# Optimization experiments

Measured on AMD Instinct MI355X. Metric: run time of the kernel, lower is better.

## Reference

```python
import jax, jax.numpy as jnp
import numpy as np

N_NODES = 20000
N_EDGES = 160000
DIM = 64          # node embedding dim
SUB = 16          # sub_dim
NB = 5            # n_bonds_type
RB = 8            # radial basis size (FeNNol default)
CUTOFF = 5.0
NLAYERS = 3
HID = 64          # conv_hidden
NSPEC = 86        # species onehot size
XI_SHAPE = RB * SUB * NB   # 640
FC_IN = XI_SHAPE + SUB     # 656
LOG2 = float(np.log(2.0))


def ssp(x):
    # shifted softplus activation
    return jax.nn.softplus(x) - jnp.asarray(LOG2, x.dtype)


def radial_bessel(r):
    # sine Bessel radial basis on [0, cutoff]; r: [E] -> [E, RB]
    n = jnp.arange(1, RB + 1, dtype=r.dtype)
    x = r[:, None]
    return jnp.sqrt(jnp.asarray(2.0 / CUTOFF, r.dtype)) * jnp.sin(n * jnp.pi * x / CUTOFF) / x


def setup_inputs() -> dict:
    key = jax.random.key(0)
    ks = jax.random.split(key, 16)
    inp = {}
    inp['species'] = jax.random.randint(ks[0], (N_NODES,), 1, NSPEC, dtype=jnp.int32)
    inp['edge_src'] = jnp.sort(jax.random.randint(ks[1], (N_EDGES,), 0, N_NODES, dtype=jnp.int32))
    inp['edge_dst'] = jax.random.randint(ks[2], (N_EDGES,), 0, N_NODES, dtype=jnp.int32)
    # distances kept away from 0 to keep 1/r finite
    inp['distances'] = jax.random.uniform(ks[3], (N_EDGES,), jnp.float32, 0.5, CUTOFF)
    inp['switch'] = jax.random.uniform(ks[4], (N_EDGES,), jnp.float32)
    inp['bond_order'] = jax.random.uniform(ks[5], (N_EDGES, NB), jnp.float32)
    s = lambda fan: 1.0 / np.sqrt(fan)
    inp['W_species'] = jax.random.normal(ks[6], (NSPEC, DIM), jnp.float32) * s(NSPEC)
    inp['Wl'] = jax.random.normal(ks[7], (NLAYERS, DIM, 2 * SUB), jnp.float32) * s(DIM)
    inp['bl'] = jnp.zeros((NLAYERS, 2 * SUB), jnp.float32)
    inp['fcW1'] = jax.random.normal(ks[8], (NLAYERS, FC_IN, HID), jnp.float32) * s(FC_IN)
    inp['fcb1'] = jnp.zeros((NLAYERS, HID), jnp.float32)
    inp['fcW2'] = jax.random.normal(ks[9], (NLAYERS, HID, HID), jnp.float32) * s(HID)
    inp['fcb2'] = jnp.zeros((NLAYERS, HID), jnp.float32)
    inp['fcW3'] = jax.random.normal(ks[10], (NLAYERS, HID, DIM), jnp.float32) * s(HID)
    inp['fcb3'] = jnp.zeros((NLAYERS, DIM), jnp.float32)
    return inp


def reference(species, edge_src, edge_dst, distances, switch, bond_order,
              W_species, Wl, bl, fcW1, fcb1, fcW2, fcb2, fcW3, fcb3):
    # onehot(species) @ W (no bias) == embedding gather
    xi = W_species[species]                      # [N, DIM]
    rb = radial_bessel(distances)                # [E, RB]
    sw = switch[:, None]                         # [E, 1]
    for l in range(NLAYERS):
        h = xi @ Wl[l] + bl[l]                   # [N, 2*SUB]
        si, mi = h[:, :SUB], h[:, SUB:]
        # per-edge outer product: [E, RB, SUB, NB] -> [E, RB*SUB*NB]
        xi_j = (rb[:, :, None, None]
                * mi[edge_dst][:, None, :, None]
                * bond_order[:, None, None, :]).reshape(N_EDGES, XI_SHAPE)
        dxi = jax.ops.segment_sum(xi_j * sw, edge_src, num_segments=N_NODES)  # [N, 640]
        dxi = jnp.concatenate([dxi, si], axis=-1)                             # [N, 656]
        dxi = ssp(dxi @ fcW1[l] + fcb1[l])
        dxi = ssp(dxi @ fcW2[l] + fcb2[l])
        dxi = dxi @ fcW3[l] + fcb3[l]            # last FC layer linear
        xi = xi + dxi
    return xi
```

## Files before the change

### kernel.cpp

```cpp
#include <hip/hip_runtime.h>
#include <math.h>

#define N_NODES 20000
#define N_EDGES 160000
#define EPAD    160256
#define NTILES  1250

#define PI_F 3.14159265358979323846f
#define LN2_F 0.69314718055994530942f

#define W1PK 43008
#define W23PK 4096
#define WPK_LAYER 51200
#define XROW 680
#define CAP 312
#define NFILL_MAX 272

#define NW_EDGE 626
#define NW_XI   625
#define NW_PACK 600
#define NW_ROW  79
#define NW_TOTAL (NW_EDGE + NW_XI + NW_PACK + NW_ROW)

typedef short short8v __attribute__((ext_vector_type(8)));
typedef float f32x4 __attribute__((ext_vector_type(4)));
typedef unsigned short u16;
typedef unsigned long long ull;

__device__ __forceinline__ float sspf(float x) {
    return fmaxf(x, 0.0f) + log1pf(expf(-fabsf(x))) - LN2_F;
}
__device__ __forceinline__ u16 f2bf(float f) {
    unsigned int u = __float_as_uint(f);
    return (u16)((u + 0x7fffu + ((u >> 16) & 1u)) >> 16);
}
__device__ __forceinline__ unsigned int pk2(float a, float b) {
    return (unsigned int)f2bf(a) | ((unsigned int)f2bf(b) << 16);
}
__device__ __forceinline__ ull mge(int t) {
    t = t < 0 ? 0 : (t > 4 ? 4 : t);
    return t == 4 ? 0ULL : (~0ULL << (t * 16));
}


__device__ void edge_wt_work(int blk, const float* __restrict__ dist,
                             const float* __restrict__ sw,
                             const float* __restrict__ bo,
                             u16* __restrict__ WT, char* smem)
{
    u16 (*tr)[264] = reinterpret_cast<u16(*)[264]>(smem);
    int tid = threadIdx.x;
    int e = blk * 256 + tid;

    if (e < N_EDGES) {
        float r = dist[e];
        float c = sqrtf(0.4f) / r * sw[e];
        float rbv[8];
        #pragma unroll
        for (int n = 0; n < 8; ++n)
            rbv[n] = c * sinf((float)(n + 1) * PI_F * r * 0.2f);
        float bov[5];
        #pragma unroll
        for (int b = 0; b < 5; ++b) bov[b] = bo[(size_t)e * 5 + b];
        #pragma unroll
        for (int n = 0; n < 8; ++n)
            #pragma unroll
            for (int b = 0; b < 5; ++b)
                tr[n * 5 + b][tid] = f2bf(rbv[n] * bov[b]);
    } else {
        #pragma unroll
        for (int j = 0; j < 40; ++j) tr[j][tid] = 0;
    }
    __syncthreads();

    #pragma unroll
    for (int i = 0; i < 5; ++i) {
        int qq = tid + i * 256;
        int s = qq >> 5, c = qq & 31;
        uint4 v = *reinterpret_cast<const uint4*>(&tr[s][c * 8]);
        *reinterpret_cast<uint4*>(WT + (size_t)s * EPAD + blk * 256 + c * 8) = v;
    }
}

__device__ void row_start_work(int blk, const int* __restrict__ src,
                               int* __restrict__ row)
{
    int i = blk * 256 + threadIdx.x;
    if (i > N_NODES) return;
    int lo = 0, hi = N_EDGES;
    while (lo < hi) {
        int mid = (lo + hi) >> 1;
        if (src[mid] < i) lo = mid + 1; else hi = mid;
    }
    row[i] = lo;
}

__device__ void pack_w_work(int blk, const float* __restrict__ fcW1,
                            const float* __restrict__ fcW2,
                            const float* __restrict__ fcW3,
                            u16* __restrict__ Wpk)
{
    int idx = blk * 256 + threadIdx.x;
    if (idx >= 3 * WPK_LAYER) return;
    int layer = idx / WPK_LAYER;
    int r = idx - layer * WPK_LAYER;
    float val = 0.0f;
    if (r < W1PK) {
        int e = r;
        int j = e & 7, lane = (e >> 3) & 63, c16 = (e >> 9) & 3, ks = e >> 11;
        int k = ks * 32 + (lane >> 4) * 8 + j;
        int colm = c16 * 16 + (lane & 15);
        if (k < 640) {
            int nbv = k >> 4, ss = k & 15;
            int nn = nbv / 5, bb = nbv - nn * 5;
            val = fcW1[(size_t)layer * 656 * 64 + (size_t)(nn * 80 + ss * 5 + bb) * 64 + colm];
        } else if (k < 656) {
            val = fcW1[(size_t)layer * 656 * 64 + (size_t)k * 64 + colm];
        }
    } else {
        bool is2 = (r < W1PK + W23PK);
        const float* W = is2 ? fcW2 : fcW3;
        int e = is2 ? (r - W1PK) : (r - W1PK - W23PK);
        int j = e & 7, lane = (e >> 3) & 63, c16 = (e >> 9) & 3, ks = e >> 11;
        int k = ks * 32 + (lane >> 4) * 8 + j;
        int colm = c16 * 16 + (lane & 15);
        val = W[(size_t)layer * 64 * 64 + (size_t)k * 64 + colm];
    }
    Wpk[(size_t)layer * WPK_LAYER + r] = f2bf(val);
}

__device__ void xi_init_h_work(int blk, const int* __restrict__ species,
                               const float* __restrict__ Wsp,
                               const float* __restrict__ Wl0,
                               const float* __restrict__ bl0,
                               float* __restrict__ xi,
                               float* __restrict__ h, char* smem)
{
    float* xs = reinterpret_cast<float*>(smem);
    float* ws = reinterpret_cast<float*>(smem + 8192);
    int tid = threadIdx.x;
    int nb = blk * 32;

    #pragma unroll
    for (int i = 0; i < 2; ++i) {
        int idx = tid + i * 256;
        int node = idx >> 4, c4 = idx & 15;
        int sp = species[nb + node];
        float4 v = reinterpret_cast<const float4*>(Wsp + (size_t)sp * 64)[c4];
        reinterpret_cast<float4*>(xs)[idx] = v;
        reinterpret_cast<float4*>(xi)[(size_t)(nb + node) * 16 + c4] = v;
    }
    {
        const float4* wsrc = reinterpret_cast<const float4*>(Wl0);
        float4* wd = reinterpret_cast<float4*>(ws);
        #pragma unroll
        for (int i = 0; i < 2; ++i) wd[tid + i * 256] = wsrc[tid + i * 256];
    }
    __syncthreads();

    int c4g = tid & 7;
    int nrow = tid >> 3;
    float4 acc = *reinterpret_cast<const float4*>(bl0 + c4g * 4);
    const float* xr = xs + nrow * 64;
    #pragma unroll 8
    for (int j = 0; j < 64; ++j) {
        float xv = xr[j];
        float4 wv = *reinterpret_cast<const float4*>(ws + j * 32 + c4g * 4);
        acc.x = fmaf(xv, wv.x, acc.x);
        acc.y = fmaf(xv, wv.y, acc.y);
        acc.z = fmaf(xv, wv.z, acc.z);
        acc.w = fmaf(xv, wv.w, acc.w);
    }
    *reinterpret_cast<float4*>(h + (size_t)(nb + nrow) * 32 + c4g * 4) = acc;
}

__global__ __launch_bounds__(256) void setup_kernel(
    const float* __restrict__ dist, const float* __restrict__ sw,
    const float* __restrict__ bo, u16* __restrict__ WT,
    const int* __restrict__ species, const float* __restrict__ Wsp,
    const float* __restrict__ Wl0, const float* __restrict__ bl0,
    float* __restrict__ xi, float* __restrict__ h0,
    const float* __restrict__ fcW1, const float* __restrict__ fcW2,
    const float* __restrict__ fcW3, u16* __restrict__ Wpk,
    const int* __restrict__ esrc, int* __restrict__ rowp)
{
    __shared__ __align__(16) char smem[21760];
    int wk = blockIdx.x;
    if (wk < NW_EDGE)
        edge_wt_work(wk, dist, sw, bo, WT, smem);
    else if (wk < NW_EDGE + NW_XI)
        xi_init_h_work(wk - NW_EDGE, species, Wsp, Wl0, bl0, xi, h0, smem);
    else if (wk < NW_EDGE + NW_XI + NW_PACK)
        pack_w_work(wk - NW_EDGE - NW_XI, fcW1, fcW2, fcW3, Wpk);
    else
        row_start_work(wk - NW_EDGE - NW_XI - NW_PACK, esrc, rowp);
}

__global__ __launch_bounds__(256) void agg_fc_fused(
    const u16* __restrict__ WT,
    const int* __restrict__ row,
    const int* __restrict__ dst,
    const float* __restrict__ h_in,
    float* __restrict__ h_out,
    const u16* __restrict__ Wpk,
    const float* __restrict__ b1,
    const float* __restrict__ b2,
    const float* __restrict__ b3,
    const float* __restrict__ Wl_next,
    const float* __restrict__ bl_next,
    int do_h,
    float* __restrict__ xi)
{
    __shared__ __align__(16) char smem[21760 + 16 * CAP * 2];
    u16 (*Xs)[XROW] = reinterpret_cast<u16(*)[XROW]>(smem);
    u16* mi  = reinterpret_cast<u16*>(smem + 21760);
    u16* Y1  = reinterpret_cast<u16*>(smem + 21760);
    u16* Y2  = reinterpret_cast<u16*>(smem + 21760 + 2304);
    float* Yo = reinterpret_cast<float*>(smem + 21760 + 4608);
    float* Wlds = reinterpret_cast<float*>(smem);
    float* Xn   = reinterpret_cast<float*>(smem + 8192);

    int tid = threadIdx.x;
    int wv = tid >> 6;
    int lane = tid & 63;
    int s = lane & 15;
    int kg = lane >> 4;
    int n0 = blockIdx.x * 16;
    int base = n0 + (wv << 2);

    int E0 = row[n0];
    int E1 = row[n0 + 16];
    int G0 = E0 & ~7;
    int nfill = E1 - G0;
    if (nfill > NFILL_MAX) nfill = NFILL_MAX;

    {
        int t = kg;
        u16* xr = &Xs[(wv << 2) + t][0];
        xr[640 + s] = f2bf(h_in[(size_t)(base + t) * 32 + s]);
        xr[656 + s] = 0;
    }

    for (int i = tid; i < nfill; i += 256) {
        int d = dst[G0 + i];
        const float4* hp = reinterpret_cast<const float4*>(h_in + (size_t)d * 32 + 16);
        float4 v0 = hp[0], v1 = hp[1], v2 = hp[2], v3 = hp[3];
        u16* col = mi + i;
        col[0 * CAP]  = f2bf(v0.x); col[1 * CAP]  = f2bf(v0.y);
        col[2 * CAP]  = f2bf(v0.z); col[3 * CAP]  = f2bf(v0.w);
        col[4 * CAP]  = f2bf(v1.x); col[5 * CAP]  = f2bf(v1.y);
        col[6 * CAP]  = f2bf(v1.z); col[7 * CAP]  = f2bf(v1.w);
        col[8 * CAP]  = f2bf(v2.x); col[9 * CAP]  = f2bf(v2.y);
        col[10 * CAP] = f2bf(v2.z); col[11 * CAP] = f2bf(v2.w);
        col[12 * CAP] = f2bf(v3.x); col[13 * CAP] = f2bf(v3.y);
        col[14 * CAP] = f2bf(v3.z); col[15 * CAP] = f2bf(v3.w);
    }
    __syncthreads();

    for (int t = 0; t < 4; ++t) {
        int node = base + t;
        int e0 = row[node], e1 = row[node + 1];
        int e0a = e0 & ~7;
        int L0 = e0a - G0;
        int nks = (e1 - e0a + 31) >> 5;

        f32x4 c0 = {0.f, 0.f, 0.f, 0.f};
        f32x4 c1 = {0.f, 0.f, 0.f, 0.f};
        f32x4 c2 = {0.f, 0.f, 0.f, 0.f};

        for (int kc = 0; kc < nks; ++kc) {
            int ebg = e0a + kc * 32 + kg * 8;
            int ebl = L0 + kc * 32 + kg * 8;
            uint4 bu = *reinterpret_cast<const uint4*>(mi + s * CAP + ebl);
            {
                int lo = e0 - ebg, hi = e1 - ebg;
                ull vA = mge(lo) & ~mge(hi);
                ull vB = mge(lo - 4) & ~mge(hi - 4);
                ull* bp = reinterpret_cast<ull*>(&bu);
                bp[0] &= vA;
                bp[1] &= vB;
            }
            short8v bfrag = *reinterpret_cast<short8v*>(&bu);
            const u16* ap = WT + (size_t)s * EPAD + ebg;
            short8v a0 = *reinterpret_cast<const short8v*>(ap);
            short8v a1 = *reinterpret_cast<const short8v*>(ap + (size_t)16 * EPAD);
            short8v a2 = *reinterpret_cast<const short8v*>(ap + (size_t)32 * EPAD);
            c0 = __builtin_amdgcn_mfma_f32_16x16x32_bf16(a0, bfrag, c0, 0, 0, 0);
            c1 = __builtin_amdgcn_mfma_f32_16x16x32_bf16(a1, bfrag, c1, 0, 0, 0);
            c2 = __builtin_amdgcn_mfma_f32_16x16x32_bf16(a2, bfrag, c2, 0, 0, 0);
        }

        u16* xr = &Xs[(wv << 2) + t][0];
        #pragma unroll
        for (int q = 0; q < 4; ++q) {
            xr[(kg * 4 + q) * 16 + s]      = f2bf(c0[q]);
            xr[(16 + kg * 4 + q) * 16 + s] = f2bf(c1[q]);
        }
        if (kg < 2) {
            #pragma unroll
            for (int q = 0; q < 4; ++q)
                xr[(32 + kg * 4 + q) * 16 + s] = f2bf(c2[q]);
        }
    }
    __syncthreads();

    int w = wv;
    int lrow = lane & 15;
    int lk = lane >> 4;
    int col = w * 16 + lrow;

    const u16* Wpk1 = Wpk;
    const u16* Wpk2 = Wpk + W1PK;
    const u16* Wpk3 = Wpk + W1PK + W23PK;

    f32x4 acc;
    {
        float bv = b1[col];
        acc[0] = bv; acc[1] = bv; acc[2] = bv; acc[3] = bv;
    }
    const u16* wp = Wpk1 + ((size_t)w * 64 + lane) * 8;
    #pragma unroll
    for (int ks = 0; ks < 21; ++ks) {
        short8v a = *reinterpret_cast<const short8v*>(&Xs[lrow][ks * 32 + lk * 8]);
        short8v b = *reinterpret_cast<const short8v*>(wp + (size_t)ks * 2048);
        acc = __builtin_amdgcn_mfma_f32_16x16x32_bf16(a, b, acc, 0, 0, 0);
    }
    __syncthreads();
    #pragma unroll
    for (int q = 0; q < 4; ++q)
        Y1[(lk * 4 + q) * 72 + col] = f2bf(sspf(acc[q]));
    __syncthreads();

    if (do_h) {
        const float4* wsrc = reinterpret_cast<const float4*>(Wl_next);
        float4* wd = reinterpret_cast<float4*>(Wlds);
        wd[tid] = wsrc[tid];
        wd[tid + 256] = wsrc[tid + 256];
    }

    {
        float bv = b2[col];
        acc[0] = bv; acc[1] = bv; acc[2] = bv; acc[3] = bv;
    }
    #pragma unroll
    for (int ks = 0; ks < 2; ++ks) {
        short8v a = *reinterpret_cast<const short8v*>(&Y1[lrow * 72 + ks * 32 + lk * 8]);
        short8v b = *reinterpret_cast<const short8v*>(Wpk2 + ((size_t)(ks * 4 + w) * 64 + lane) * 8);
        acc = __builtin_amdgcn_mfma_f32_16x16x32_bf16(a, b, acc, 0, 0, 0);
    }
    __syncthreads();
    #pragma unroll
    for (int q = 0; q < 4; ++q)
        Y2[(lk * 4 + q) * 72 + col] = f2bf(sspf(acc[q]));
    __syncthreads();

    {
        float bv = b3[col];
        acc[0] = bv; acc[1] = bv; acc[2] = bv; acc[3] = bv;
    }
    #pragma unroll
    for (int ks = 0; ks < 2; ++ks) {
        short8v a = *reinterpret_cast<const short8v*>(&Y2[lrow * 72 + ks * 32 + lk * 8]);
        short8v b = *reinterpret_cast<const short8v*>(Wpk3 + ((size_t)(ks * 4 + w) * 64 + lane) * 8);
        acc = __builtin_amdgcn_mfma_f32_16x16x32_bf16(a, b, acc, 0, 0, 0);
    }
    #pragma unroll
    for (int q = 0; q < 4; ++q)
        Yo[(lk * 4 + q) * 68 + col] = acc[q];
    __syncthreads();

    {
        int rr = tid >> 4;
        int cc = tid & 15;
        float4 dv = *reinterpret_cast<const float4*>(Yo + rr * 68 + cc * 4);
        float4* xpn = reinterpret_cast<float4*>(xi + (size_t)(n0 + rr) * 64 + cc * 4);
        float4 o = *xpn;
        o.x += dv.x; o.y += dv.y; o.z += dv.z; o.w += dv.w;
        *xpn = o;
        if (do_h)
            *reinterpret_cast<float4*>(Xn + rr * 68 + cc * 4) = o;
    }

    if (do_h) {
        __syncthreads();
        int node = tid >> 4;
        int c2 = (tid & 15) * 2;
        const float* xnr = Xn + node * 68;
        float h0 = bl_next[c2], h1 = bl_next[c2 + 1];
        #pragma unroll 8
        for (int j = 0; j < 64; ++j) {
            float xv = xnr[j];
            h0 = fmaf(xv, Wlds[j * 32 + c2], h0);
            h1 = fmaf(xv, Wlds[j * 32 + c2 + 1], h1);
        }
        *reinterpret_cast<float2*>(h_out + (size_t)(n0 + node) * 32 + c2) =
            make_float2(h0, h1);
    }
}

extern "C" void kernel_launch(void* const* d_in, const int* in_sizes, int n_in,
                              void* d_out, int out_size, void* d_ws, size_t ws_size,
                              hipStream_t stream) {
    const int*   species = (const int*)d_in[0];
    const int*   esrc    = (const int*)d_in[1];
    const int*   edst    = (const int*)d_in[2];
    const float* dist    = (const float*)d_in[3];
    const float* sw      = (const float*)d_in[4];
    const float* bo      = (const float*)d_in[5];
    const float* Wsp     = (const float*)d_in[6];
    const float* Wl      = (const float*)d_in[7];
    const float* bl      = (const float*)d_in[8];
    const float* fcW1    = (const float*)d_in[9];
    const float* fcb1    = (const float*)d_in[10];
    const float* fcW2    = (const float*)d_in[11];
    const float* fcb2    = (const float*)d_in[12];
    const float* fcW3    = (const float*)d_in[13];
    const float* fcb3    = (const float*)d_in[14];
    float* xi = (float*)d_out;

    char* ws = (char*)d_ws;
    u16*   WT   = (u16*)ws;
    int*   rowp = (int*)(ws + 15384576);
    float* h0   = (float*)(ws + 15464704);
    float* h1   = (float*)(ws + 18024704);
    u16*   Wpk  = (u16*)(ws + 20584704);

    hipLaunchKernelGGL(setup_kernel, dim3(NW_TOTAL), dim3(256), 0, stream,
                       dist, sw, bo, WT,
                       species, Wsp, Wl, bl, xi, h0,
                       fcW1, fcW2, fcW3, Wpk,
                       esrc, rowp);

    float* hbuf[2] = {h0, h1};
    for (int l = 0; l < 3; ++l) {
        int do_h = (l < 2) ? 1 : 0;
        int lnext = do_h ? (l + 1) : l;
        hipLaunchKernelGGL(agg_fc_fused, dim3(NTILES), dim3(256), 0, stream,
                           WT, rowp, edst,
                           hbuf[l & 1], hbuf[(l + 1) & 1],
                           Wpk + (size_t)l * WPK_LAYER,
                           fcb1 + (size_t)l * 64, fcb2 + (size_t)l * 64,
                           fcb3 + (size_t)l * 64,
                           Wl + (size_t)lnext * 64 * 32,
                           bl + (size_t)lnext * 32,
                           do_h, xi);
    }
}
```

Baseline: 96.17 us.

## Store edge basis weights in edge-group-major layout and use sine recurrence

The per-edge radial-times-bond weight table is now stored in groups of 8 edges. Each group holds all 40 feature rows, padded to 48, in one contiguous 768-byte block, replacing the old feature-major layout with stride EPAD. The MFMA A-fragment loads in the aggregation kernel then hit contiguous memory rather than rows far apart, which should improve coalescing and cache-line use. The setup also replaces the eight sinf calls with one fast sincos plus a Chebyshev recurrence. That recurrence may slightly change rounding in the bf16-stored weights.

```diff
diff --git a/kernel.cpp b/kernel.cpp
--- a/kernel.cpp
+++ b/kernel.cpp
@@ -4,6 +4,8 @@
 #define N_NODES 20000
 #define N_EDGES 160000
 #define EPAD    160256
+#define NGROUPS (EPAD / 8)
+#define GSTRIDE 384
 #define NTILES  1250
 
 #define PI_F 3.14159265358979323846f
@@ -42,11 +44,10 @@
     return t == 4 ? 0ULL : (~0ULL << (t * 16));
 }
 
-
 __device__ void edge_wt_work(int blk, const float* __restrict__ dist,
                              const float* __restrict__ sw,
                              const float* __restrict__ bo,
-                             u16* __restrict__ WT, char* smem)
+                             u16* __restrict__ WTg, char* smem)
 {
     u16 (*tr)[264] = reinterpret_cast<u16(*)[264]>(smem);
     int tid = threadIdx.x;
@@ -55,10 +56,21 @@
     if (e < N_EDGES) {
         float r = dist[e];
         float c = sqrtf(0.4f) / r * sw[e];
+        float th = PI_F * r * 0.2f;
+        float s1, c1;
+        __sincosf(th, &s1, &c1);
+        float k2c = 2.0f * c1;
         float rbv[8];
-        #pragma unroll
-        for (int n = 0; n < 8; ++n)
-            rbv[n] = c * sinf((float)(n + 1) * PI_F * r * 0.2f);
+        rbv[0] = s1;
+        float sp = 0.0f, sc = s1;
+        #pragma unroll
+        for (int n = 1; n < 8; ++n) {
+            float sn = k2c * sc - sp;
+            rbv[n] = sn;
+            sp = sc; sc = sn;
+        }
+        #pragma unroll
+        for (int n = 0; n < 8; ++n) rbv[n] *= c;
         float bov[5];
         #pragma unroll
         for (int b = 0; b < 5; ++b) bov[b] = bo[(size_t)e * 5 + b];
@@ -74,11 +86,13 @@
     __syncthreads();
 
     #pragma unroll
-    for (int i = 0; i < 5; ++i) {
-        int qq = tid + i * 256;
-        int s = qq >> 5, c = qq & 31;
-        uint4 v = *reinterpret_cast<const uint4*>(&tr[s][c * 8]);
-        *reinterpret_cast<uint4*>(WT + (size_t)s * EPAD + blk * 256 + c * 8) = v;
+    for (int i = 0; i < 6; ++i) {
+        int r = i * 8 + (tid & 7);
+        int gl = tid >> 3;
+        uint4 v = make_uint4(0u, 0u, 0u, 0u);
+        if (r < 40) v = *reinterpret_cast<const uint4*>(&tr[r][gl * 8]);
+        *reinterpret_cast<uint4*>(
+            WTg + ((size_t)(blk * 32 + gl) * GSTRIDE + r * 8)) = v;
     }
 }
 
@@ -176,7 +190,7 @@
 
 __global__ __launch_bounds__(256) void setup_kernel(
     const float* __restrict__ dist, const float* __restrict__ sw,
-    const float* __restrict__ bo, u16* __restrict__ WT,
+    const float* __restrict__ bo, u16* __restrict__ WTg,
     const int* __restrict__ species, const float* __restrict__ Wsp,
     const float* __restrict__ Wl0, const float* __restrict__ bl0,
     float* __restrict__ xi, float* __restrict__ h0,
@@ -187,7 +201,7 @@
     __shared__ __align__(16) char smem[21760];
     int wk = blockIdx.x;
     if (wk < NW_EDGE)
-        edge_wt_work(wk, dist, sw, bo, WT, smem);
+        edge_wt_work(wk, dist, sw, bo, WTg, smem);
     else if (wk < NW_EDGE + NW_XI)
         xi_init_h_work(wk - NW_EDGE, species, Wsp, Wl0, bl0, xi, h0, smem);
     else if (wk < NW_EDGE + NW_XI + NW_PACK)
@@ -197,7 +211,7 @@
 }
 
 __global__ __launch_bounds__(256) void agg_fc_fused(
-    const u16* __restrict__ WT,
+    const u16* __restrict__ WTg,
     const int* __restrict__ row,
     const int* __restrict__ dst,
     const float* __restrict__ h_in,
@@ -281,10 +295,10 @@
                 bp[1] &= vB;
             }
             short8v bfrag = *reinterpret_cast<short8v*>(&bu);
-            const u16* ap = WT + (size_t)s * EPAD + ebg;
-            short8v a0 = *reinterpret_cast<const short8v*>(ap);
-            short8v a1 = *reinterpret_cast<const short8v*>(ap + (size_t)16 * EPAD);
-            short8v a2 = *reinterpret_cast<const short8v*>(ap + (size_t)32 * EPAD);
+            const u16* gp = WTg + (size_t)(ebg >> 3) * GSTRIDE + (size_t)s * 8;
+            short8v a0 = *reinterpret_cast<const short8v*>(gp);
+            short8v a1 = *reinterpret_cast<const short8v*>(gp + 128);
+            short8v a2 = *reinterpret_cast<const short8v*>(gp + 256);
             c0 = __builtin_amdgcn_mfma_f32_16x16x32_bf16(a0, bfrag, c0, 0, 0, 0);
             c1 = __builtin_amdgcn_mfma_f32_16x16x32_bf16(a1, bfrag, c1, 0, 0, 0);
             c2 = __builtin_amdgcn_mfma_f32_16x16x32_bf16(a2, bfrag, c2, 0, 0, 0);
@@ -419,14 +433,14 @@
     float* xi = (float*)d_out;
 
     char* ws = (char*)d_ws;
-    u16*   WT   = (u16*)ws;
+    u16*   WTg  = (u16*)ws;
     int*   rowp = (int*)(ws + 15384576);
     float* h0   = (float*)(ws + 15464704);
     float* h1   = (float*)(ws + 18024704);
     u16*   Wpk  = (u16*)(ws + 20584704);
 
     hipLaunchKernelGGL(setup_kernel, dim3(NW_TOTAL), dim3(256), 0, stream,
-                       dist, sw, bo, WT,
+                       dist, sw, bo, WTg,
                        species, Wsp, Wl, bl, xi, h0,
                        fcW1, fcW2, fcW3, Wpk,
                        esrc, rowp);
@@ -436,7 +450,7 @@
         int do_h = (l < 2) ? 1 : 0;
         int lnext = do_h ? (l + 1) : l;
         hipLaunchKernelGGL(agg_fc_fused, dim3(NTILES), dim3(256), 0, stream,
-                           WT, rowp, edst,
+                           WTg, rowp, edst,
                            hbuf[l & 1], hbuf[(l + 1) & 1],
                            Wpk + (size_t)l * WPK_LAYER,
                            fcb1 + (size_t)l * 64, fcb2 + (size_t)l * 64,
```

New measurement: 87.32 us. -9.2%, faster.
